# Optimization experiments

Hardware: AMD Instinct MI355X
Metric: run time of the kernel (lower is better)

Reference implementation:

```python
import jax, jax.numpy as jnp
import numpy as np

B, T, V, H, O = 256, 1024, 128, 128, 2  # batch, max_len, input_size, hidden, n_outputs


def setup_inputs() -> dict:
    key = jax.random.key(0)
    ks = jax.random.split(key, 9)
    # ragged one-hot sequences: symbol 0 is the pad symbol
    lengths = jax.random.randint(ks[0], (B,), 1, T + 1)
    symbols = jax.random.randint(ks[1], (B, T), 1, V)  # real symbols in [1, V)
    t_idx = jnp.arange(T)[None, :]
    symbols = jnp.where(t_idx < lengths[:, None], symbols, 0)  # pad tail with symbol 0
    x = jax.nn.one_hot(symbols, V, dtype=jnp.float32)  # [B, T, V]
    # RNN params (torch nn.RNN layout: W_ih [H, V-1], W_hh [H, H])
    s = 1.0 / np.sqrt(H)
    W_ih = jax.random.uniform(ks[2], (H, V - 1), minval=-s, maxval=s)
    W_hh = jax.random.uniform(ks[3], (H, H), minval=-s, maxval=s)
    b_ih = jax.random.uniform(ks[4], (H,), minval=-s, maxval=s)
    b_hh = jax.random.uniform(ks[5], (H,), minval=-s, maxval=s)
    # dense head: Linear(H, O)
    W_out = jax.random.uniform(ks[6], (O, H), minval=-s, maxval=s)
    b_out = jax.random.uniform(ks[7], (O,), minval=-s, maxval=s)
    return {"x": x, "W_ih": W_ih, "W_hh": W_hh, "b_ih": b_ih,
            "b_hh": b_hh, "W_out": W_out, "b_out": b_out}


def reference(x, W_ih, W_hh, b_ih, b_hh, W_out, b_out):
    Bk, Tk, Vk = x.shape
    # unpad: length = first timestep whose argmax is the pad symbol (index 0)
    is_pad = jnp.argmax(x, axis=-1) == 0  # [B, T]
    length = jnp.where(is_pad.any(-1), jnp.argmax(is_pad, axis=-1), Tk)  # [B]
    active = jnp.arange(Tk)[None, :] < length[:, None]  # [B, T]
    feats = x[..., 1:]  # strip pad column -> [B, T, V-1]
    # precompute input projection for all timesteps (streaming part)
    pre = jnp.einsum('btf,hf->bth', feats, W_ih) + b_ih + b_hh  # [B, T, H]

    def step(h, inp):
        pre_t, act_t = inp  # [B, H], [B]
        h_new = jnp.tanh(pre_t + h @ W_hh.T)
        h = jnp.where(act_t[:, None], h_new, h)  # freeze hidden past each seq's length
        return h, None

    h0 = jnp.zeros((Bk, W_hh.shape[0]), dtype=x.dtype)
    h_last, _ = jax.lax.scan(step, h0, (pre.transpose(1, 0, 2), active.T))
    fed = jax.nn.softmax(h_last @ W_out.T + b_out, axis=-1)  # [B, O]
    hidden = h_last[None]  # [1, B, H], matches torch stacked layer hidden
    return fed, hidden
```

## Files before the change

### kernel.cpp

```cpp
#include <hip/hip_runtime.h>
#include <stdint.h>

#define Bsz   256
#define Tlen  1024
#define Vocab 128
#define Hdim  128
#define NTHR  512
#define WTN   ((Vocab - 1) * Hdim)

typedef _Float16 half2_t __attribute__((ext_vector_type(2)));

#define HCHB  48
#define HBUFI (8 * HCHB / 4)

__device__ __forceinline__ float tanh_fast(float x) {
    float e = __builtin_amdgcn_exp2f(x * 2.885390081777927f);
    return 1.0f - 2.0f * __builtin_amdgcn_rcpf(e + 1.0f);
}

__device__ __forceinline__ float dpp_xor1(float s) {
    return __int_as_float(__builtin_amdgcn_mov_dpp(__float_as_int(s), 0xB1, 0xF, 0xF, true));
}
__device__ __forceinline__ float dpp_xor2(float s) {
    return __int_as_float(__builtin_amdgcn_mov_dpp(__float_as_int(s), 0x4E, 0xF, 0xF, true));
}
__device__ __forceinline__ float dpp_hm(float s) {
    return __int_as_float(__builtin_amdgcn_mov_dpp(__float_as_int(s), 0x141, 0xF, 0xF, true));
}

__global__ __launch_bounds__(256) void transpose_kernel(
    const float* __restrict__ W_ih, float* __restrict__ wt)
{
    int idx = blockIdx.x * 256 + threadIdx.x;
    if (idx < WTN) {
        int h = idx / (Vocab - 1);
        int f = idx - h * (Vocab - 1);
        wt[f * Hdim + h] = W_ih[idx];
    }
}

__global__ __launch_bounds__(NTHR, 2) void rnn_kernel(
    const float* __restrict__ x, const float* __restrict__ wt,
    const float* __restrict__ W_hh,
    const float* __restrict__ b_ih, const float* __restrict__ b_hh,
    const float* __restrict__ W_out, const float* __restrict__ b_out,
    float* __restrict__ out)
{
    __shared__ float wt_s[WTN];
    __shared__ int   syms[Tlen];
    __shared__ __align__(16) int hbuf[2][HBUFI];
    __shared__ int   len_sh;

    const int tid = threadIdx.x;
    const int b   = blockIdx.x;
    const int g   = tid >> 3;
    const int j   = tid & 7;

    if (tid == 0) len_sh = Tlen;
    for (int k = tid; k < 2 * HBUFI; k += NTHR) ((int*)hbuf)[k] = 0;

    int wp[16];
    #pragma unroll
    for (int r = 0; r < 2; r++) {
        const float4* wrow = (const float4*)(W_hh + (2 * g + r) * Hdim + 16 * j);
        #pragma unroll
        for (int q4 = 0; q4 < 4; q4++) {
            float4 t4 = wrow[q4];
            wp[r * 8 + q4 * 2 + 0] = __builtin_bit_cast(int, __builtin_amdgcn_cvt_pkrtz(t4.x, t4.y));
            wp[r * 8 + q4 * 2 + 1] = __builtin_bit_cast(int, __builtin_amdgcn_cvt_pkrtz(t4.z, t4.w));
        }
    }
    const float bias0 = b_ih[2 * g]     + b_hh[2 * g];
    const float bias1 = b_ih[2 * g + 1] + b_hh[2 * g + 1];

    {
        const float4* src = (const float4*)wt;
        float4* dst = (float4*)wt_s;
        for (int k = tid; k < WTN / 4; k += NTHR) dst[k] = src[k];
    }

    const float4* xb = (const float4*)(x + (size_t)b * Tlen * Vocab);
    for (int k = tid; k < (Tlen * Vocab) / 4; k += NTHR) {
        float4 v = xb[k];
        int c = -1;
        if      (v.x > 0.5f) c = 0;
        else if (v.y > 0.5f) c = 1;
        else if (v.z > 0.5f) c = 2;
        else if (v.w > 0.5f) c = 3;
        if (c >= 0) syms[k >> 5] = ((k & 31) << 2) + c;
    }
    __syncthreads();

    {
        int lm = Tlen;
        for (int k = tid; k < Tlen; k += NTHR)
            if (syms[k] == 0 && k < lm) lm = k;
        if (lm < Tlen) atomicMin(&len_sh, lm);
    }
    __syncthreads();
    const int len = len_sh;

    const float2* wt2 = (const float2*)wt_s;
    float2 pre_v = {0.0f, 0.0f}, p_t1 = {0.0f, 0.0f};
    int s_t2 = 1;
    if (len > 0) pre_v = wt2[(syms[0] - 1) * 64 + g];
    if (len > 1) p_t1  = wt2[(syms[1] - 1) * 64 + g];
    if (len > 2) s_t2  = syms[2];

    const char* hb0 = (const char*)hbuf[0];
    const char* hb1 = (const char*)hbuf[1];
    const int roff = j * HCHB;
    const int woff = (g >> 3) * HCHB + ((2 * g) & 15) * 2;

    for (int t = 0; t < len; t++) {
        #pragma unroll
        for (int k = 0; k < 16; k += 8)
            asm volatile("" : "+v"(wp[k]), "+v"(wp[k+1]), "+v"(wp[k+2]), "+v"(wp[k+3]),
                             "+v"(wp[k+4]), "+v"(wp[k+5]), "+v"(wp[k+6]), "+v"(wp[k+7]));

        float2 p_t2 = wt2[(s_t2 - 1) * 64 + g];
        int   s_t3 = (t + 3 < len) ? syms[t + 3] : 1;

        const char* hb = (t & 1) ? hb1 : hb0;
        uint4 r0 = *(const uint4*)(hb + roff);
        uint4 r1 = *(const uint4*)(hb + roff + 16);
        unsigned hr[8] = {r0.x, r0.y, r0.z, r0.w, r1.x, r1.y, r1.z, r1.w};

        float a0 = 0.0f, a1 = 0.0f;
        #pragma unroll
        for (int p = 0; p < 8; p++) {
            half2_t hh = __builtin_bit_cast(half2_t, hr[p]);
            a0 = __builtin_amdgcn_fdot2(hh, __builtin_bit_cast(half2_t, wp[p]),     a0, false);
            a1 = __builtin_amdgcn_fdot2(hh, __builtin_bit_cast(half2_t, wp[8 + p]), a1, false);
        }
        a0 += dpp_xor1(a0); a1 += dpp_xor1(a1);
        a0 += dpp_xor2(a0); a1 += dpp_xor2(a1);
        a0 += dpp_hm(a0);   a1 += dpp_hm(a1);

        if (j == 0) {
            float h0 = tanh_fast(a0 + pre_v.x + bias0);
            float h1 = tanh_fast(a1 + pre_v.y + bias1);
            int pk = __builtin_bit_cast(int, __builtin_amdgcn_cvt_pkrtz(h0, h1));
            *(int*)(((char*)hbuf[(t + 1) & 1]) + woff) = pk;
        }
        pre_v = p_t1; p_t1 = p_t2; s_t2 = s_t3;
        __syncthreads();
    }

    const _Float16* hf = (const _Float16*)hbuf[len & 1];
    #define HGET(e) ((float)hf[((e) >> 4) * 24 + ((e) & 15)])
    if (tid < Hdim)
        out[2 * Bsz + b * Hdim + tid] = HGET(tid);
    if (tid < 64) {
        float h0 = HGET(tid);
        float h1 = HGET(tid + 64);
        float p0 = W_out[tid] * h0 + W_out[64 + tid] * h1;
        float p1 = W_out[128 + tid] * h0 + W_out[192 + tid] * h1;
        #pragma unroll
        for (int off = 32; off > 0; off >>= 1) {
            p0 += __shfl_down(p0, off, 64);
            p1 += __shfl_down(p1, off, 64);
        }
        if (tid == 0) {
            float l0 = p0 + b_out[0], l1 = p1 + b_out[1];
            float m  = fmaxf(l0, l1);
            float e0 = __expf(l0 - m), e1 = __expf(l1 - m);
            float d  = e0 + e1;
            out[b * 2 + 0] = e0 / d;
            out[b * 2 + 1] = e1 / d;
        }
    }
    #undef HGET
}

extern "C" void kernel_launch(void* const* d_in, const int* in_sizes, int n_in,
                              void* d_out, int out_size, void* d_ws, size_t ws_size,
                              hipStream_t stream) {
    const float* x     = (const float*)d_in[0];
    const float* W_ih  = (const float*)d_in[1];
    const float* W_hh  = (const float*)d_in[2];
    const float* b_ih  = (const float*)d_in[3];
    const float* b_hh  = (const float*)d_in[4];
    const float* W_out = (const float*)d_in[5];
    const float* b_out = (const float*)d_in[6];
    float* out = (float*)d_out;

    float* wt = (float*)d_ws;

    const int NTRN = (WTN + 255) / 256;
    transpose_kernel<<<NTRN, 256, 0, stream>>>(W_ih, wt);
    rnn_kernel<<<Bsz, NTHR, 0, stream>>>(x, wt, W_hh, b_ih, b_hh, W_out, b_out, out);
}
```

Before: 527.9 us.

## Run recurrence in a single wavefront with register-resident W_hh, no barriers

The serial recurrence now runs on one 64-lane wavefront instead of 512 threads. Each lane holds four half-precision W_hh row halves in registers (128 VGPRs), and lane pairs combine their partial sums with a single DPP exchange. This removes the per-timestep __syncthreads and the double-buffered hidden state, leaving one LDS buffer that the same wave reads and then writes. The biases are folded into the pre-transposed input projection in the prep kernel. The cost is a much longer serial dot-product chain per lane and high register pressure under the launch bounds, which may cause spills.

New measurement: 595.2 us. 1.13x slower.

```diff
diff --git a/kernel.cpp b/kernel.cpp
--- a/kernel.cpp
+++ b/kernel.cpp
@@ -10,9 +10,6 @@
 
 typedef _Float16 half2_t __attribute__((ext_vector_type(2)));
 
-#define HCHB  48
-#define HBUFI (8 * HCHB / 4)
-
 __device__ __forceinline__ float tanh_fast(float x) {
     float e = __builtin_amdgcn_exp2f(x * 2.885390081777927f);
     return 1.0f - 2.0f * __builtin_amdgcn_rcpf(e + 1.0f);
@@ -21,60 +18,37 @@
 __device__ __forceinline__ float dpp_xor1(float s) {
     return __int_as_float(__builtin_amdgcn_mov_dpp(__float_as_int(s), 0xB1, 0xF, 0xF, true));
 }
-__device__ __forceinline__ float dpp_xor2(float s) {
-    return __int_as_float(__builtin_amdgcn_mov_dpp(__float_as_int(s), 0x4E, 0xF, 0xF, true));
-}
-__device__ __forceinline__ float dpp_hm(float s) {
-    return __int_as_float(__builtin_amdgcn_mov_dpp(__float_as_int(s), 0x141, 0xF, 0xF, true));
-}
 
-__global__ __launch_bounds__(256) void transpose_kernel(
-    const float* __restrict__ W_ih, float* __restrict__ wt)
+__global__ __launch_bounds__(256) void prep_kernel(
+    const float* __restrict__ W_ih, const float* __restrict__ b_ih,
+    const float* __restrict__ b_hh, float* __restrict__ wtb)
 {
     int idx = blockIdx.x * 256 + threadIdx.x;
     if (idx < WTN) {
         int h = idx / (Vocab - 1);
         int f = idx - h * (Vocab - 1);
-        wt[f * Hdim + h] = W_ih[idx];
+        wtb[f * Hdim + h] = W_ih[idx] + b_ih[h] + b_hh[h];
     }
 }
 
 __global__ __launch_bounds__(NTHR, 2) void rnn_kernel(
-    const float* __restrict__ x, const float* __restrict__ wt,
-    const float* __restrict__ W_hh,
-    const float* __restrict__ b_ih, const float* __restrict__ b_hh,
-    const float* __restrict__ W_out, const float* __restrict__ b_out,
-    float* __restrict__ out)
+    const float* __restrict__ x, const float* __restrict__ wtb,
+    const float* __restrict__ W_hh, const float* __restrict__ W_out,
+    const float* __restrict__ b_out, float* __restrict__ out)
 {
     __shared__ float wt_s[WTN];
     __shared__ int   syms[Tlen];
-    __shared__ __align__(16) int hbuf[2][HBUFI];
+    __shared__ __align__(16) int hbuf[Hdim / 2];
     __shared__ int   len_sh;
 
     const int tid = threadIdx.x;
     const int b   = blockIdx.x;
-    const int g   = tid >> 3;
-    const int j   = tid & 7;
 
     if (tid == 0) len_sh = Tlen;
-    for (int k = tid; k < 2 * HBUFI; k += NTHR) ((int*)hbuf)[k] = 0;
-
-    int wp[16];
-    #pragma unroll
-    for (int r = 0; r < 2; r++) {
-        const float4* wrow = (const float4*)(W_hh + (2 * g + r) * Hdim + 16 * j);
-        #pragma unroll
-        for (int q4 = 0; q4 < 4; q4++) {
-            float4 t4 = wrow[q4];
-            wp[r * 8 + q4 * 2 + 0] = __builtin_bit_cast(int, __builtin_amdgcn_cvt_pkrtz(t4.x, t4.y));
-            wp[r * 8 + q4 * 2 + 1] = __builtin_bit_cast(int, __builtin_amdgcn_cvt_pkrtz(t4.z, t4.w));
-        }
-    }
-    const float bias0 = b_ih[2 * g]     + b_hh[2 * g];
-    const float bias1 = b_ih[2 * g + 1] + b_hh[2 * g + 1];
+    if (tid < Hdim / 2) hbuf[tid] = 0;
 
     {
-        const float4* src = (const float4*)wt;
+        const float4* src = (const float4*)wtb;
         float4* dst = (float4*)wt_s;
         for (int k = tid; k < WTN / 4; k += NTHR) dst[k] = src[k];
     }
@@ -100,77 +74,93 @@
     __syncthreads();
     const int len = len_sh;
 
+    if (tid >= 64) return;
+
+    const int l = tid;
+    const int g = l >> 1;
+    const int j = l & 1;
+
+    int wp[128];
+    {
+        const int rows[4] = {4 * g + 2 * j, 4 * g + 2 * j + 1,
+                             4 * g + 2 - 2 * j, 4 * g + 3 - 2 * j};
+        #pragma unroll
+        for (int rs = 0; rs < 4; rs++) {
+            const float4* wrow = (const float4*)(W_hh + rows[rs] * Hdim + 64 * j);
+            #pragma unroll
+            for (int q = 0; q < 16; q++) {
+                float4 t4 = wrow[q];
+                wp[rs * 32 + 2 * q]     = __builtin_bit_cast(int, __builtin_amdgcn_cvt_pkrtz(t4.x, t4.y));
+                wp[rs * 32 + 2 * q + 1] = __builtin_bit_cast(int, __builtin_amdgcn_cvt_pkrtz(t4.z, t4.w));
+            }
+        }
+    }
+
     const float2* wt2 = (const float2*)wt_s;
     float2 pre_v = {0.0f, 0.0f}, p_t1 = {0.0f, 0.0f};
     int s_t2 = 1;
-    if (len > 0) pre_v = wt2[(syms[0] - 1) * 64 + g];
-    if (len > 1) p_t1  = wt2[(syms[1] - 1) * 64 + g];
+    if (len > 0) pre_v = wt2[(syms[0] - 1) * 64 + l];
+    if (len > 1) p_t1  = wt2[(syms[1] - 1) * 64 + l];
     if (len > 2) s_t2  = syms[2];
 
-    const char* hb0 = (const char*)hbuf[0];
-    const char* hb1 = (const char*)hbuf[1];
-    const int roff = j * HCHB;
-    const int woff = (g >> 3) * HCHB + ((2 * g) & 15) * 2;
+    const char* hbp = (const char*)hbuf + 128 * j;
 
     for (int t = 0; t < len; t++) {
         #pragma unroll
-        for (int k = 0; k < 16; k += 8)
+        for (int k = 0; k < 128; k += 8)
             asm volatile("" : "+v"(wp[k]), "+v"(wp[k+1]), "+v"(wp[k+2]), "+v"(wp[k+3]),
-                             "+v"(wp[k+4]), "+v"(wp[k+5]), "+v"(wp[k+6]), "+v"(wp[k+7]));
+                              "+v"(wp[k+4]), "+v"(wp[k+5]), "+v"(wp[k+6]), "+v"(wp[k+7]));
 
-        float2 p_t2 = wt2[(s_t2 - 1) * 64 + g];
+        float2 p_t2 = wt2[(s_t2 - 1) * 64 + l];
         int   s_t3 = (t + 3 < len) ? syms[t + 3] : 1;
 
-        const char* hb = (t & 1) ? hb1 : hb0;
-        uint4 r0 = *(const uint4*)(hb + roff);
-        uint4 r1 = *(const uint4*)(hb + roff + 16);
-        unsigned hr[8] = {r0.x, r0.y, r0.z, r0.w, r1.x, r1.y, r1.z, r1.w};
+        uint4 q0 = *(const uint4*)(hbp);
+        uint4 q1 = *(const uint4*)(hbp + 16);
+        uint4 q2 = *(const uint4*)(hbp + 32);
+        uint4 q3 = *(const uint4*)(hbp + 48);
+        uint4 q4 = *(const uint4*)(hbp + 64);
+        uint4 q5 = *(const uint4*)(hbp + 80);
+        uint4 q6 = *(const uint4*)(hbp + 96);
+        uint4 q7 = *(const uint4*)(hbp + 112);
+        unsigned hr[32] = {q0.x, q0.y, q0.z, q0.w, q1.x, q1.y, q1.z, q1.w,
+                           q2.x, q2.y, q2.z, q2.w, q3.x, q3.y, q3.z, q3.w,
+                           q4.x, q4.y, q4.z, q4.w, q5.x, q5.y, q5.z, q5.w,
+                           q6.x, q6.y, q6.z, q6.w, q7.x, q7.y, q7.z, q7.w};
 
-        float a0 = 0.0f, a1 = 0.0f;
+        float a0 = pre_v.x, a1 = pre_v.y, a2 = 0.0f, a3 = 0.0f;
         #pragma unroll
-        for (int p = 0; p < 8; p++) {
-            half2_t hh = __builtin_bit_cast(half2_t, hr[p]);
-            a0 = __builtin_amdgcn_fdot2(hh, __builtin_bit_cast(half2_t, wp[p]),     a0, false);
-            a1 = __builtin_amdgcn_fdot2(hh, __builtin_bit_cast(half2_t, wp[8 + p]), a1, false);
+        for (int d = 0; d < 32; d++) {
+            half2_t hh = __builtin_bit_cast(half2_t, hr[d]);
+            a0 = __builtin_amdgcn_fdot2(hh, __builtin_bit_cast(half2_t, wp[d]),       a0, false);
+            a1 = __builtin_amdgcn_fdot2(hh, __builtin_bit_cast(half2_t, wp[32 + d]),  a1, false);
+            a2 = __builtin_amdgcn_fdot2(hh, __builtin_bit_cast(half2_t, wp[64 + d]),  a2, false);
+            a3 = __builtin_amdgcn_fdot2(hh, __builtin_bit_cast(half2_t, wp[96 + d]),  a3, false);
         }
-        a0 += dpp_xor1(a0); a1 += dpp_xor1(a1);
-        a0 += dpp_xor2(a0); a1 += dpp_xor2(a1);
-        a0 += dpp_hm(a0);   a1 += dpp_hm(a1);
-
-        if (j == 0) {
-            float h0 = tanh_fast(a0 + pre_v.x + bias0);
-            float h1 = tanh_fast(a1 + pre_v.y + bias1);
-            int pk = __builtin_bit_cast(int, __builtin_amdgcn_cvt_pkrtz(h0, h1));
-            *(int*)(((char*)hbuf[(t + 1) & 1]) + woff) = pk;
-        }
+        float h0 = tanh_fast(a0 + dpp_xor1(a2));
+        float h1 = tanh_fast(a1 + dpp_xor1(a3));
+        hbuf[l] = __builtin_bit_cast(int, __builtin_amdgcn_cvt_pkrtz(h0, h1));
         pre_v = p_t1; p_t1 = p_t2; s_t2 = s_t3;
-        __syncthreads();
     }
 
-    const _Float16* hf = (const _Float16*)hbuf[len & 1];
-    #define HGET(e) ((float)hf[((e) >> 4) * 24 + ((e) & 15)])
-    if (tid < Hdim)
-        out[2 * Bsz + b * Hdim + tid] = HGET(tid);
-    if (tid < 64) {
-        float h0 = HGET(tid);
-        float h1 = HGET(tid + 64);
-        float p0 = W_out[tid] * h0 + W_out[64 + tid] * h1;
-        float p1 = W_out[128 + tid] * h0 + W_out[192 + tid] * h1;
-        #pragma unroll
-        for (int off = 32; off > 0; off >>= 1) {
-            p0 += __shfl_down(p0, off, 64);
-            p1 += __shfl_down(p1, off, 64);
-        }
-        if (tid == 0) {
-            float l0 = p0 + b_out[0], l1 = p1 + b_out[1];
-            float m  = fmaxf(l0, l1);
-            float e0 = __expf(l0 - m), e1 = __expf(l1 - m);
-            float d  = e0 + e1;
-            out[b * 2 + 0] = e0 / d;
-            out[b * 2 + 1] = e1 / d;
-        }
+    half2_t hv = __builtin_bit_cast(half2_t, hbuf[l]);
+    float h0 = (float)hv.x, h1 = (float)hv.y;
+    *(float2*)(out + 2 * Bsz + b * Hdim + 2 * l) = make_float2(h0, h1);
+
+    float p0 = W_out[2 * l] * h0 + W_out[2 * l + 1] * h1;
+    float p1 = W_out[Hdim + 2 * l] * h0 + W_out[Hdim + 2 * l + 1] * h1;
+    #pragma unroll
+    for (int off = 32; off > 0; off >>= 1) {
+        p0 += __shfl_down(p0, off, 64);
+        p1 += __shfl_down(p1, off, 64);
     }
-    #undef HGET
+    if (l == 0) {
+        float l0 = p0 + b_out[0], l1 = p1 + b_out[1];
+        float m  = fmaxf(l0, l1);
+        float e0 = __expf(l0 - m), e1 = __expf(l1 - m);
+        float d  = e0 + e1;
+        out[b * 2 + 0] = e0 / d;
+        out[b * 2 + 1] = e1 / d;
+    }
 }
 
 extern "C" void kernel_launch(void* const* d_in, const int* in_sizes, int n_in,
@@ -185,9 +175,9 @@
     const float* b_out = (const float*)d_in[6];
     float* out = (float*)d_out;
 
-    float* wt = (float*)d_ws;
+    float* wtb = (float*)d_ws;
 
     const int NTRN = (WTN + 255) / 256;
-    transpose_kernel<<<NTRN, 256, 0, stream>>>(W_ih, wt);
-    rnn_kernel<<<Bsz, NTHR, 0, stream>>>(x, wt, W_hh, b_ih, b_hh, W_out, b_out, out);
+    prep_kernel<<<NTRN, 256, 0, stream>>>(W_ih, b_ih, b_hh, wtb);
+    rnn_kernel<<<Bsz, NTHR, 0, stream>>>(x, wtb, W_hh, W_out, b_out, out);
 }
```

## Halve RNN block to 256 threads with 4 lanes per hidden pair

Applied to the files above, without the earlier changes.

The recurrent kernel now uses 256 threads per block instead of 512. Each group of 4 lanes covers two hidden units over 32 columns, holding 32 packed fp16 weights in registers and using split accumulators, and one DPP reduction stage is dropped. The shared hidden-state buffer layout is reorganized to match, and the one-hot scan batches eight float4 loads per thread before decoding them. The aim is to cut per-step barrier cost and reduction depth on the serial critical path. The trade-offs are more register pressure, more LDS reads per lane each step, and one block per CU.

Result: faster. 453.5 us (median of 2 runs) (-14.1%).

```diff
diff --git a/kernel.cpp b/kernel.cpp
--- a/kernel.cpp
+++ b/kernel.cpp
@@ -5,13 +5,13 @@
 #define Tlen  1024
 #define Vocab 128
 #define Hdim  128
-#define NTHR  512
+#define NTHR  256
 #define WTN   ((Vocab - 1) * Hdim)
 
+#define CHD   20
+#define HBUFI (4 * CHD)
+
 typedef _Float16 half2_t __attribute__((ext_vector_type(2)));
-
-#define HCHB  48
-#define HBUFI (8 * HCHB / 4)
 
 __device__ __forceinline__ float tanh_fast(float x) {
     float e = __builtin_amdgcn_exp2f(x * 2.885390081777927f);
@@ -23,9 +23,6 @@
 }
 __device__ __forceinline__ float dpp_xor2(float s) {
     return __int_as_float(__builtin_amdgcn_mov_dpp(__float_as_int(s), 0x4E, 0xF, 0xF, true));
-}
-__device__ __forceinline__ float dpp_hm(float s) {
-    return __int_as_float(__builtin_amdgcn_mov_dpp(__float_as_int(s), 0x141, 0xF, 0xF, true));
 }
 
 __global__ __launch_bounds__(256) void transpose_kernel(
@@ -39,7 +36,7 @@
     }
 }
 
-__global__ __launch_bounds__(NTHR, 2) void rnn_kernel(
+__global__ __launch_bounds__(NTHR, 1) void rnn_kernel(
     const float* __restrict__ x, const float* __restrict__ wt,
     const float* __restrict__ W_hh,
     const float* __restrict__ b_ih, const float* __restrict__ b_hh,
@@ -53,21 +50,21 @@
 
     const int tid = threadIdx.x;
     const int b   = blockIdx.x;
-    const int g   = tid >> 3;
-    const int j   = tid & 7;
+    const int g   = tid >> 2;
+    const int j   = tid & 3;
 
     if (tid == 0) len_sh = Tlen;
-    for (int k = tid; k < 2 * HBUFI; k += NTHR) ((int*)hbuf)[k] = 0;
-
-    int wp[16];
+    if (tid < 2 * HBUFI) ((int*)hbuf)[tid] = 0;
+
+    int wp[32];
     #pragma unroll
     for (int r = 0; r < 2; r++) {
-        const float4* wrow = (const float4*)(W_hh + (2 * g + r) * Hdim + 16 * j);
-        #pragma unroll
-        for (int q4 = 0; q4 < 4; q4++) {
+        const float4* wrow = (const float4*)(W_hh + (2 * g + r) * Hdim + 32 * j);
+        #pragma unroll
+        for (int q4 = 0; q4 < 8; q4++) {
             float4 t4 = wrow[q4];
-            wp[r * 8 + q4 * 2 + 0] = __builtin_bit_cast(int, __builtin_amdgcn_cvt_pkrtz(t4.x, t4.y));
-            wp[r * 8 + q4 * 2 + 1] = __builtin_bit_cast(int, __builtin_amdgcn_cvt_pkrtz(t4.z, t4.w));
+            wp[r * 16 + q4 * 2 + 0] = __builtin_bit_cast(int, __builtin_amdgcn_cvt_pkrtz(t4.x, t4.y));
+            wp[r * 16 + q4 * 2 + 1] = __builtin_bit_cast(int, __builtin_amdgcn_cvt_pkrtz(t4.z, t4.w));
         }
     }
     const float bias0 = b_ih[2 * g]     + b_hh[2 * g];
@@ -79,15 +76,24 @@
         for (int k = tid; k < WTN / 4; k += NTHR) dst[k] = src[k];
     }
 
-    const float4* xb = (const float4*)(x + (size_t)b * Tlen * Vocab);
-    for (int k = tid; k < (Tlen * Vocab) / 4; k += NTHR) {
-        float4 v = xb[k];
-        int c = -1;
-        if      (v.x > 0.5f) c = 0;
-        else if (v.y > 0.5f) c = 1;
-        else if (v.z > 0.5f) c = 2;
-        else if (v.w > 0.5f) c = 3;
-        if (c >= 0) syms[k >> 5] = ((k & 31) << 2) + c;
+    {
+        const float4* xb = (const float4*)(x + (size_t)b * Tlen * Vocab);
+        const int R4 = Tlen * Vocab / 4;
+        for (int base = 0; base < R4; base += NTHR * 8) {
+            float4 v[8];
+            #pragma unroll
+            for (int i = 0; i < 8; i++) v[i] = xb[base + NTHR * i + tid];
+            #pragma unroll
+            for (int i = 0; i < 8; i++) {
+                int k = base + NTHR * i + tid;
+                int c = -1;
+                if      (v[i].x > 0.5f) c = 0;
+                else if (v[i].y > 0.5f) c = 1;
+                else if (v[i].z > 0.5f) c = 2;
+                else if (v[i].w > 0.5f) c = 3;
+                if (c >= 0) syms[k >> 5] = ((k & 31) << 2) + c;
+            }
+        }
     }
     __syncthreads();
 
@@ -109,46 +115,52 @@
 
     const char* hb0 = (const char*)hbuf[0];
     const char* hb1 = (const char*)hbuf[1];
-    const int roff = j * HCHB;
-    const int woff = (g >> 3) * HCHB + ((2 * g) & 15) * 2;
+    const int roff = j * (CHD * 4);
+    const int widx = CHD * (g >> 4) + (g & 15);
 
     for (int t = 0; t < len; t++) {
         #pragma unroll
-        for (int k = 0; k < 16; k += 8)
+        for (int k = 0; k < 32; k += 8)
             asm volatile("" : "+v"(wp[k]), "+v"(wp[k+1]), "+v"(wp[k+2]), "+v"(wp[k+3]),
-                             "+v"(wp[k+4]), "+v"(wp[k+5]), "+v"(wp[k+6]), "+v"(wp[k+7]));
-
-        float2 p_t2 = wt2[(s_t2 - 1) * 64 + g];
-        int   s_t3 = (t + 3 < len) ? syms[t + 3] : 1;
+                              "+v"(wp[k+4]), "+v"(wp[k+5]), "+v"(wp[k+6]), "+v"(wp[k+7]));
 
         const char* hb = (t & 1) ? hb1 : hb0;
         uint4 r0 = *(const uint4*)(hb + roff);
         uint4 r1 = *(const uint4*)(hb + roff + 16);
-        unsigned hr[8] = {r0.x, r0.y, r0.z, r0.w, r1.x, r1.y, r1.z, r1.w};
-
-        float a0 = 0.0f, a1 = 0.0f;
-        #pragma unroll
-        for (int p = 0; p < 8; p++) {
-            half2_t hh = __builtin_bit_cast(half2_t, hr[p]);
-            a0 = __builtin_amdgcn_fdot2(hh, __builtin_bit_cast(half2_t, wp[p]),     a0, false);
-            a1 = __builtin_amdgcn_fdot2(hh, __builtin_bit_cast(half2_t, wp[8 + p]), a1, false);
-        }
+        uint4 r2 = *(const uint4*)(hb + roff + 32);
+        uint4 r3 = *(const uint4*)(hb + roff + 48);
+
+        float2 p_t2 = wt2[(s_t2 - 1) * 64 + g];
+        int   s_t3 = (t + 3 < len) ? syms[t + 3] : 1;
+
+        unsigned hr[16] = {r0.x, r0.y, r0.z, r0.w, r1.x, r1.y, r1.z, r1.w,
+                           r2.x, r2.y, r2.z, r2.w, r3.x, r3.y, r3.z, r3.w};
+
+        float a00 = 0.0f, a01 = 0.0f, a10 = 0.0f, a11 = 0.0f;
+        #pragma unroll
+        for (int d = 0; d < 8; d++) {
+            half2_t h0 = __builtin_bit_cast(half2_t, hr[d]);
+            half2_t h1 = __builtin_bit_cast(half2_t, hr[8 + d]);
+            a00 = __builtin_amdgcn_fdot2(h0, __builtin_bit_cast(half2_t, wp[d]),      a00, false);
+            a01 = __builtin_amdgcn_fdot2(h1, __builtin_bit_cast(half2_t, wp[8 + d]),  a01, false);
+            a10 = __builtin_amdgcn_fdot2(h0, __builtin_bit_cast(half2_t, wp[16 + d]), a10, false);
+            a11 = __builtin_amdgcn_fdot2(h1, __builtin_bit_cast(half2_t, wp[24 + d]), a11, false);
+        }
+        float a0 = a00 + a01, a1 = a10 + a11;
         a0 += dpp_xor1(a0); a1 += dpp_xor1(a1);
         a0 += dpp_xor2(a0); a1 += dpp_xor2(a1);
-        a0 += dpp_hm(a0);   a1 += dpp_hm(a1);
-
-        if (j == 0) {
-            float h0 = tanh_fast(a0 + pre_v.x + bias0);
-            float h1 = tanh_fast(a1 + pre_v.y + bias1);
-            int pk = __builtin_bit_cast(int, __builtin_amdgcn_cvt_pkrtz(h0, h1));
-            *(int*)(((char*)hbuf[(t + 1) & 1]) + woff) = pk;
-        }
+
+        float h0 = tanh_fast(a0 + pre_v.x + bias0);
+        float h1 = tanh_fast(a1 + pre_v.y + bias1);
+        int pk = __builtin_bit_cast(int, __builtin_amdgcn_cvt_pkrtz(h0, h1));
+        if (j == 0) ((int*)hbuf[(t + 1) & 1])[widx] = pk;
+
         pre_v = p_t1; p_t1 = p_t2; s_t2 = s_t3;
         __syncthreads();
     }
 
     const _Float16* hf = (const _Float16*)hbuf[len & 1];
-    #define HGET(e) ((float)hf[((e) >> 4) * 24 + ((e) & 15)])
+    #define HGET(e) ((float)hf[40 * ((e) >> 5) + (((e) >> 1) & 15) * 2 + ((e) & 1)])
     if (tid < Hdim)
         out[2 * Bsz + b * Hdim + tid] = HGET(tid);
     if (tid < 64) {
```
